# Performance work log

Measured on AMD Instinct MI355X. Metric: run time of the kernel, lower is better.

Reference implementation:

```python
import jax, jax.numpy as jnp
import numpy as np

B, L, D_MODEL = 4, 4096, 128
D_INNER, D_STATE, DT_RANK, D_CONV = 256, 16, 8, 4
EPS = 1e-5


def setup_inputs() -> dict:
    key = jax.random.key(0)
    ks = jax.random.split(key, 10)
    s = lambda *sh: 0.02
    inp = {
        'x': jax.random.normal(ks[0], (B, L, D_MODEL), jnp.float32),
        'norm_w': jnp.ones((D_MODEL,), jnp.float32),
        # Linear weights stored as (in, out) so y = x @ W
        'in_proj_w': jax.random.normal(ks[1], (D_MODEL, 2 * D_INNER), jnp.float32) * 0.02,
        'conv_w': jax.random.normal(ks[2], (D_INNER, D_CONV), jnp.float32) * 0.2,
        'conv_b': jnp.zeros((D_INNER,), jnp.float32),
        'x_proj_w': jax.random.normal(ks[3], (D_INNER, DT_RANK + 2 * D_STATE), jnp.float32) * 0.02,
        'dt_proj_w': jax.random.normal(ks[4], (DT_RANK, D_INNER), jnp.float32) * 0.1,
        'dt_proj_b': jnp.zeros((D_INNER,), jnp.float32),
        'A_log': jnp.log(jnp.tile(jnp.arange(1, D_STATE + 1, dtype=jnp.float32)[None, :], (D_INNER, 1))),
        'D': jnp.ones((D_INNER,), jnp.float32),
        'out_proj_w': jax.random.normal(ks[5], (D_INNER, D_MODEL), jnp.float32) * 0.02,
    }
    return inp


def _mamba_block(x, norm_w, in_proj_w, conv_w, conv_b, x_proj_w,
                 dt_proj_w, dt_proj_b, A_log, D, out_proj_w):
    b, l, d = x.shape
    # RMSNorm
    h = x * jax.lax.rsqrt(jnp.mean(x * x, axis=-1, keepdims=True) + EPS) * norm_w
    # in_proj -> split into x path and residual gate
    xr = h @ in_proj_w                      # (b, l, 2*d_inner)
    xi, res = jnp.split(xr, 2, axis=-1)
    # depthwise causal conv1d over time
    xc = jnp.transpose(xi, (0, 2, 1))       # (b, d_inner, l)
    kernel = conv_w[:, None, :]             # (d_inner, 1, d_conv)
    xc = jax.lax.conv_general_dilated(
        xc, kernel, window_strides=(1,), padding=[(D_CONV - 1, 0)],
        feature_group_count=D_INNER,
        dimension_numbers=('NCH', 'OIH', 'NCH')) + conv_b[None, :, None]
    xc = jnp.transpose(xc, (0, 2, 1))       # (b, l, d_inner)
    xc = jax.nn.silu(xc)
    # SSM parameterization
    A = -jnp.exp(A_log.astype(jnp.float32))           # (d_inner, n)
    x_dbl = xc @ x_proj_w                              # (b, l, dt_rank + 2n)
    delta = x_dbl[..., :DT_RANK]
    Bmat = x_dbl[..., DT_RANK:DT_RANK + D_STATE]       # (b, l, n)
    Cmat = x_dbl[..., DT_RANK + D_STATE:]              # (b, l, n)
    delta = jax.nn.softplus(delta @ dt_proj_w + dt_proj_b)  # (b, l, d_inner)
    # discretize
    deltaA = jnp.exp(jnp.einsum('bld,dn->bldn', delta, A))  # (b, l, d_inner, n)
    deltaB_u = delta[..., None] * Bmat[:, :, None, :] * xc[..., None]
    # selective scan over time (lax.scan replaces the Python loop)
    def step(s, inputs):
        dA_t, dBu_t, C_t = inputs
        s = dA_t * s + dBu_t                     # (b, d_inner, n)
        y_t = jnp.einsum('bdn,bn->bd', s, C_t)   # (b, d_inner)
        return s, y_t
    s0 = jnp.zeros((b, D_INNER, D_STATE), xc.dtype)
    scan_in = (jnp.transpose(deltaA, (1, 0, 2, 3)),
               jnp.transpose(deltaB_u, (1, 0, 2, 3)),
               jnp.transpose(Cmat, (1, 0, 2)))
    _, ys = jax.lax.scan(step, s0, scan_in)      # (l, b, d_inner)
    y = jnp.transpose(ys, (1, 0, 2)) + xc * D    # (b, l, d_inner)
    y = y * jax.nn.silu(res)
    return y @ out_proj_w + x                    # residual add


def reference(x, norm_w, in_proj_w, conv_w, conv_b, x_proj_w,
              dt_proj_w, dt_proj_b, A_log, D, out_proj_w):
    return _mamba_block(x, norm_w, in_proj_w, conv_w, conv_b, x_proj_w,
                        dt_proj_w, dt_proj_b, A_log, D, out_proj_w)
```

## Files before the change

kernel.cpp:

```cpp
#include <hip/hip_runtime.h>
#include <math.h>

#define B_    4
#define L_    4096
#define DM    128
#define DI    256
#define DS    16
#define DTR   8
#define XPN   (DTR + 2*DS)
#define NB    (DI + 2*DS)
#define M_    (B_*L_)
#define CHUNK 32
#define NC    (L_/CHUNK)
#define LOG2E 1.4426950408889634f
#define PREP_N (512*128 + NB*DI + DM*DI)

typedef __attribute__((ext_vector_type(8))) short bf16x8;
typedef __attribute__((ext_vector_type(4))) float f32x4;
typedef unsigned short ushort_t;

__device__ __forceinline__ ushort_t f2bf(float f) {
  unsigned int u = __float_as_uint(f);
  u += 0x7FFFu + ((u >> 16) & 1u);
  return (ushort_t)(u >> 16);
}
__device__ __forceinline__ float bf2f(ushort_t u) {
  return __uint_as_float(((unsigned int)u) << 16);
}

__global__ __launch_bounds__(256) void prep_rms_kernel(const float* __restrict__ x,
                                                       const float* __restrict__ nw,
                                                       const float* __restrict__ inW,
                                                       const float* __restrict__ Wx,
                                                       const float* __restrict__ Wdt,
                                                       const float* __restrict__ outw,
                                                       ushort_t* __restrict__ xbf,
                                                       ushort_t* __restrict__ inWt,
                                                       ushort_t* __restrict__ WbigT,
                                                       ushort_t* __restrict__ outWt) {
  if (blockIdx.x < M_ / 4) {
    int row  = blockIdx.x * 4 + (threadIdx.x >> 6);
    int lane = threadIdx.x & 63;
    const float* xp = x + (size_t)row * DM;
    float v0 = xp[lane], v1 = xp[lane + 64];
    float s = v0 * v0 + v1 * v1;
    #pragma unroll
    for (int off = 32; off > 0; off >>= 1) s += __shfl_xor(s, off);
    float r = rsqrtf(s / DM + 1e-5f);
    ushort_t* op = xbf + (size_t)row * DM;
    op[lane]      = f2bf(v0 * r * nw[lane]);
    op[lane + 64] = f2bf(v1 * r * nw[lane + 64]);
    return;
  }
  int g = (blockIdx.x - M_ / 4) * 256 + threadIdx.x;
  if (g < 512 * 128) {
    int n = g >> 7, k = g & 127;
    inWt[g] = f2bf(inW[k * 512 + n]);
  } else if (g < 512 * 128 + NB * DI) {
    int q = g - 512 * 128;
    int c = q >> 8, k = q & 255;
    float v;
    if (c < DI) {
      v = 0.f;
      #pragma unroll
      for (int j = 0; j < DTR; ++j) v = fmaf(Wx[k * XPN + j], Wdt[j * DI + c], v);
    } else {
      v = Wx[k * XPN + DTR + (c - DI)];
    }
    WbigT[q] = f2bf(v);
  } else if (g < PREP_N) {
    int q = g - (512 * 128 + NB * DI);
    int n = q >> 8, k = q & 255;
    outWt[q] = f2bf(outw[k * DM + n]);
  }
}

__global__ __launch_bounds__(256) void g1_conv_kernel(const ushort_t* __restrict__ A,
                                                      const ushort_t* __restrict__ Wt,
                                                      const float* __restrict__ cw,
                                                      const float* __restrict__ cb,
                                                      ushort_t* __restrict__ xcbf,
                                                      ushort_t* __restrict__ resbf) {
  constexpr int KK = 128, NT = 4;
  __shared__ __align__(16) char smem_raw[35648];
  ushort_t (*Asm)[145][8] = (ushort_t (*)[145][8])smem_raw;
  ushort_t (*Bx)[65][8]   = (ushort_t (*)[65][8])(smem_raw + 18560);
  ushort_t (*Br)[65][8]   = (ushort_t (*)[65][8])(smem_raw + 26880);
  float* T = (float*)smem_raw;
  const int tid  = threadIdx.x;
  const int wave = tid >> 6, lane = tid & 63;
  const int quad = lane >> 4, l16 = lane & 15;
  const int row0 = blockIdx.x * 128;
  const int by   = blockIdx.y;
  const int c0x  = by * 64;
  const int c0r  = 256 + by * 64;
  const bool zpad = (row0 & (L_ - 1)) == 0;
  f32x4 ax[2][NT], ar[2][NT], acc2[NT];
  #pragma unroll
  for (int mt = 0; mt < 2; ++mt)
    #pragma unroll
    for (int nt = 0; nt < NT; ++nt) {
      ax[mt][nt] = (f32x4){0.f, 0.f, 0.f, 0.f};
      ar[mt][nt] = (f32x4){0.f, 0.f, 0.f, 0.f};
    }
  #pragma unroll
  for (int nt = 0; nt < NT; ++nt) acc2[nt] = (f32x4){0.f, 0.f, 0.f, 0.f};

  for (int k0 = 0; k0 < KK; k0 += 64) {
    #pragma unroll
    for (int i = 0; i < 5; ++i) {
      int q = tid + i * 256;
      if (i < 4 || tid < 128) {
        int m = q >> 3, kb = q & 7;
        bf16x8 v = {0, 0, 0, 0, 0, 0, 0, 0};
        if (!(zpad && m < 16))
          v = *(const bf16x8*)(A + (size_t)(row0 - 16 + m) * KK + k0 + kb * 8);
        *(bf16x8*)(&Asm[kb][m][0]) = v;
      }
    }
    #pragma unroll
    for (int i = 0; i < 2; ++i) {
      int q = tid + i * 256;
      int n = q >> 3, kb = q & 7;
      *(bf16x8*)(&Bx[kb][n][0]) =
          *(const bf16x8*)(Wt + (size_t)(c0x + n) * KK + k0 + kb * 8);
    }
    #pragma unroll
    for (int i = 0; i < 2; ++i) {
      int q = tid + i * 256;
      int n = q >> 3, kb = q & 7;
      *(bf16x8*)(&Br[kb][n][0]) =
          *(const bf16x8*)(Wt + (size_t)(c0r + n) * KK + k0 + kb * 8);
    }
    __syncthreads();
    #pragma unroll
    for (int ks = 0; ks < 2; ++ks) {
      bf16x8 af[2], bx[NT], br[NT];
      #pragma unroll
      for (int mt = 0; mt < 2; ++mt)
        af[mt] = *(const bf16x8*)(&Asm[ks * 4 + quad][16 + wave * 32 + mt * 16 + l16][0]);
      #pragma unroll
      for (int nt = 0; nt < NT; ++nt) {
        bx[nt] = *(const bf16x8*)(&Bx[ks * 4 + quad][nt * 16 + l16][0]);
        br[nt] = *(const bf16x8*)(&Br[ks * 4 + quad][nt * 16 + l16][0]);
      }
      #pragma unroll
      for (int mt = 0; mt < 2; ++mt)
        #pragma unroll
        for (int nt = 0; nt < NT; ++nt) {
          ax[mt][nt] = __builtin_amdgcn_mfma_f32_16x16x32_bf16(af[mt], bx[nt],
                                                               ax[mt][nt], 0, 0, 0);
          ar[mt][nt] = __builtin_amdgcn_mfma_f32_16x16x32_bf16(af[mt], br[nt],
                                                               ar[mt][nt], 0, 0, 0);
        }
      if (wave == 0) {
        bf16x8 ab = *(const bf16x8*)(&Asm[ks * 4 + quad][l16][0]);
        #pragma unroll
        for (int nt = 0; nt < NT; ++nt)
          acc2[nt] = __builtin_amdgcn_mfma_f32_16x16x32_bf16(ab, bx[nt],
                                                             acc2[nt], 0, 0, 0);
      }
    }
    __syncthreads();
  }

  #pragma unroll
  for (int mt = 0; mt < 2; ++mt)
    #pragma unroll
    for (int nt = 0; nt < NT; ++nt) {
      int col   = c0x + nt * 16 + l16;
      int rbase = row0 + wave * 32 + mt * 16 + quad * 4;
      #pragma unroll
      for (int r = 0; r < 4; ++r)
        resbf[(size_t)(rbase + r) * DI + col] = f2bf(ar[mt][nt][r]);
    }

  #pragma unroll
  for (int mt = 0; mt < 2; ++mt)
    #pragma unroll
    for (int nt = 0; nt < NT; ++nt)
      #pragma unroll
      for (int r = 0; r < 4; ++r)
        T[(3 + wave * 32 + mt * 16 + quad * 4 + r) * 68 + nt * 16 + l16] =
            ax[mt][nt][r];
  if (wave == 0 && quad == 3) {
    #pragma unroll
    for (int nt = 0; nt < NT; ++nt)
      #pragma unroll
      for (int r = 1; r < 4; ++r)
        T[(r - 1) * 68 + nt * 16 + l16] = acc2[nt][r];
  }
  __syncthreads();
  {
    const int c   = tid & 63;
    const int R0  = (tid >> 6) * 32;
    const int dch = c0x + c;
    float4 w4   = *(const float4*)(cw + dch * 4);
    float bias  = cb[dch];
    float t0 = T[(R0 + 0) * 68 + c];
    float t1 = T[(R0 + 1) * 68 + c];
    float t2 = T[(R0 + 2) * 68 + c];
    for (int rr = 0; rr < 32; ++rr) {
      float t3 = T[(R0 + rr + 3) * 68 + c];
      float s = fmaf(w4.x, t0, fmaf(w4.y, t1, fmaf(w4.z, t2, fmaf(w4.w, t3, bias))));
      float v = s / (1.f + __expf(-s));
      xcbf[(size_t)(row0 + R0 + rr) * DI + dch] = f2bf(v);
      t0 = t1; t1 = t2; t2 = t3;
    }
  }
}

__global__ __launch_bounds__(512, 4) void scanA_kernel(
    const ushort_t* __restrict__ xcbf, const ushort_t* __restrict__ WbigT,
    const float* __restrict__ bdt, const float* __restrict__ Alog,
    ushort_t* __restrict__ deltab, ushort_t* __restrict__ Bmb,
    ushort_t* __restrict__ Cmb, float2* __restrict__ PS) {
  __shared__ __align__(16) ushort_t Asm[32][33][8];
  __shared__ float T[32][257];
  __shared__ float Bs[32][17], Cs[32][17];
  const int tid  = threadIdx.x;
  const int wave = tid >> 6, lane = tid & 63;
  const int quad = lane >> 4, l16 = lane & 15;
  const int b = blockIdx.x >> 7, c = blockIdx.x & (NC - 1);
  const size_t rowbase = (size_t)b * L_ + (size_t)c * CHUNK;
  const int d  = (wave << 5) | (lane & 31);
  const int nh = lane >> 5;
  const int n0 = nh * 8;

  {
    int m = tid & 31, kb = tid >> 5;
    *(bf16x8*)(&Asm[kb][m][0]) =
        *(const bf16x8*)(xcbf + (rowbase + m) * DI + kb * 8);
    *(bf16x8*)(&Asm[kb + 16][m][0]) =
        *(const bf16x8*)(xcbf + (rowbase + m) * DI + (kb + 16) * 8);
  }
  __syncthreads();

  for (int tp = wave; tp < 36; tp += 8) {
    int mt = tp / 18, nt = tp % 18;
    f32x4 acc = {0.f, 0.f, 0.f, 0.f};
    #pragma unroll
    for (int ks = 0; ks < 8; ++ks) {
      bf16x8 af = *(const bf16x8*)(&Asm[ks * 4 + quad][mt * 16 + l16][0]);
      bf16x8 bf = *(const bf16x8*)(WbigT + (size_t)(nt * 16 + l16) * DI + ks * 32 + quad * 8);
      acc = __builtin_amdgcn_mfma_f32_16x16x32_bf16(af, bf, acc, 0, 0, 0);
    }
    int row = mt * 16 + quad * 4;
    if (nt < 16) {
      int col = nt * 16 + l16;
      float bb = bdt[col];
      #pragma unroll
      for (int r = 0; r < 4; ++r) {
        float v = acc[r] + bb;
        T[row + r][col] = (v > 20.f) ? v : log1pf(__expf(v));
      }
    } else if (nt == 16) {
      #pragma unroll
      for (int r = 0; r < 4; ++r) Bs[row + r][l16] = acc[r];
    } else {
      #pragma unroll
      for (int r = 0; r < 4; ++r) Cs[row + r][l16] = acc[r];
    }
  }
  __syncthreads();

  #pragma unroll
  for (int i = 0; i < 8; ++i) {
    int idx2 = tid + i * 512;
    int row = idx2 >> 7, cp = idx2 & 127;
    unsigned int pk = (unsigned int)f2bf(T[row][2 * cp]) |
                      ((unsigned int)f2bf(T[row][2 * cp + 1]) << 16);
    *(unsigned int*)(deltab + (rowbase + row) * DI + 2 * cp) = pk;
  }
  {
    int row = tid >> 4, n = tid & 15;
    Bmb[rowbase * DS + tid] = f2bf(Bs[row][n]);
    Cmb[rowbase * DS + tid] = f2bf(Cs[row][n]);
  }

  float c0 = -__expf(Alog[d * DS]) * LOG2E;
  float aln[8];
  #pragma unroll
  for (int j = 0; j < 8; ++j) aln[j] = -__expf(Alog[d * DS + n0 + j]) * LOG2E;
  bool geom = true;
  #pragma unroll
  for (int j = 0; j < 8; ++j)
    geom = geom && (fabsf(aln[j] - (n0 + j + 1) * c0) <= 1e-3f * fabsf(aln[j]));

  float P[8], S[8];
  #pragma unroll
  for (int j = 0; j < 8; ++j) { P[j] = 1.f; S[j] = 0.f; }
  for (int t = 0; t < CHUNK; ++t) {
    float dl = T[t][d];
    float xv = bf2f(Asm[d >> 3][t][d & 7]);
    float du = dl * xv;
    if (geom) {
      float e1 = exp2f(dl * c0);
      float a;
      if (nh) { float e2 = e1 * e1, e4 = e2 * e2; a = e4 * e4 * e1; }
      else a = e1;
      #pragma unroll
      for (int j = 0; j < 8; ++j) {
        P[j] *= a;
        S[j] = fmaf(a, S[j], du * Bs[t][n0 + j]);
        a *= e1;
      }
    } else {
      #pragma unroll
      for (int j = 0; j < 8; ++j) {
        float a = exp2f(dl * aln[j]);
        P[j] *= a;
        S[j] = fmaf(a, S[j], du * Bs[t][n0 + j]);
      }
    }
  }
  size_t ob = ((size_t)(b * NC + c) << 12) + ((nh * 256 + d) << 3);
  float4* p4 = (float4*)(PS + ob);
  p4[0] = make_float4(P[0], S[0], P[1], S[1]);
  p4[1] = make_float4(P[2], S[2], P[3], S[3]);
  p4[2] = make_float4(P[4], S[4], P[5], S[5]);
  p4[3] = make_float4(P[6], S[6], P[7], S[7]);
}

__global__ __launch_bounds__(64) void scanB_kernel(const float2* __restrict__ PS,
                                                   float* __restrict__ sinit) {
  int g  = blockIdx.x * 64 + threadIdx.x;
  int b  = g >> 12;
  int dn = g & 4095;
  float s = 0.f;
  #pragma unroll 16
  for (int c = 0; c < NC; ++c) {
    size_t idx = ((size_t)(b * NC + c) << 12) + dn;
    sinit[idx] = s;
    float2 v = PS[idx];
    s = fmaf(v.x, s, v.y);
  }
}

__global__ __launch_bounds__(512, 4) void scanC_kernel(
    const ushort_t* __restrict__ deltab, const ushort_t* __restrict__ xcbf,
    const ushort_t* __restrict__ Bmb, const ushort_t* __restrict__ Cmb,
    const float* __restrict__ Alog, const float* __restrict__ Dp,
    const ushort_t* __restrict__ resbf, const float* __restrict__ sinit,
    const ushort_t* __restrict__ outWt, const float* __restrict__ x,
    float* __restrict__ out) {
  __shared__ float Bs[32][17], Cs[32][17];
  __shared__ __align__(16) ushort_t y2s[32][264];
  const int tid  = threadIdx.x;
  const int wave = tid >> 6, lane = tid & 63;
  const int quad = lane >> 4, l16 = lane & 15;
  const int b = blockIdx.x >> 7, c = blockIdx.x & (NC - 1);
  const size_t rowbase = (size_t)b * L_ + (size_t)c * CHUNK;
  const int d  = (wave << 5) | (lane & 31);
  const int nh = lane >> 5;
  const int n0 = nh * 8;
  {
    int row = tid >> 4, n = tid & 15;
    Bs[row][n] = bf2f(Bmb[rowbase * DS + tid]);
    Cs[row][n] = bf2f(Cmb[rowbase * DS + tid]);
  }
  float c0 = -__expf(Alog[d * DS]) * LOG2E;
  float aln[8];
  #pragma unroll
  for (int j = 0; j < 8; ++j) aln[j] = -__expf(Alog[d * DS + n0 + j]) * LOG2E;
  bool geom = true;
  #pragma unroll
  for (int j = 0; j < 8; ++j)
    geom = geom && (fabsf(aln[j] - (n0 + j + 1) * c0) <= 1e-3f * fabsf(aln[j]));
  const float Dd = Dp[d];
  float S[8];
  {
    size_t ib = ((size_t)(b * NC + c) << 12) + ((nh * 256 + d) << 3);
    float4 v0 = *(const float4*)(sinit + ib);
    float4 v1 = *(const float4*)(sinit + ib + 4);
    S[0] = v0.x; S[1] = v0.y; S[2] = v0.z; S[3] = v0.w;
    S[4] = v1.x; S[5] = v1.y; S[6] = v1.z; S[7] = v1.w;
  }
  __syncthreads();
  for (int t = 0; t < CHUNK; ++t) {
    float dl = bf2f(deltab[(rowbase + t) * DI + d]);
    float xv = bf2f(xcbf[(rowbase + t) * DI + d]);
    float du = dl * xv;
    float y = 0.f;
    if (geom) {
      float e1 = exp2f(dl * c0);
      float a;
      if (nh) { float e2 = e1 * e1, e4 = e2 * e2; a = e4 * e4 * e1; }
      else a = e1;
      #pragma unroll
      for (int j = 0; j < 8; ++j) {
        S[j] = fmaf(a, S[j], du * Bs[t][n0 + j]);
        y = fmaf(S[j], Cs[t][n0 + j], y);
        a *= e1;
      }
    } else {
      #pragma unroll
      for (int j = 0; j < 8; ++j) {
        float a = exp2f(dl * aln[j]);
        S[j] = fmaf(a, S[j], du * Bs[t][n0 + j]);
        y = fmaf(S[j], Cs[t][n0 + j], y);
      }
    }
    float yo = __shfl_xor(y, 32);
    if (nh == 0) {
      float rv = bf2f(resbf[(rowbase + t) * DI + d]);
      float yt = y + yo + xv * Dd;
      float sil = rv / (1.f + __expf(-rv));
      y2s[t][d] = f2bf(yt * sil);
    }
  }
  __syncthreads();
  #pragma unroll
  for (int mt = 0; mt < 2; ++mt) {
    f32x4 acc = {0.f, 0.f, 0.f, 0.f};
    #pragma unroll
    for (int ks = 0; ks < 8; ++ks) {
      bf16x8 af = *(const bf16x8*)(&y2s[mt * 16 + l16][ks * 32 + quad * 8]);
      bf16x8 bf = *(const bf16x8*)(outWt + (size_t)(wave * 16 + l16) * DI + ks * 32 + quad * 8);
      acc = __builtin_amdgcn_mfma_f32_16x16x32_bf16(af, bf, acc, 0, 0, 0);
    }
    int col = wave * 16 + l16;
    size_t rb = rowbase + mt * 16 + quad * 4;
    #pragma unroll
    for (int r = 0; r < 4; ++r)
      out[(rb + r) * DM + col] = acc[r] + x[(rb + r) * DM + col];
  }
}

extern "C" void kernel_launch(void* const* d_in, const int* in_sizes, int n_in,
                              void* d_out, int out_size, void* d_ws, size_t ws_size,
                              hipStream_t stream) {
  const float* x      = (const float*)d_in[0];
  const float* norm_w = (const float*)d_in[1];
  const float* inW    = (const float*)d_in[2];
  const float* convw  = (const float*)d_in[3];
  const float* convb  = (const float*)d_in[4];
  const float* xprojw = (const float*)d_in[5];
  const float* dtw    = (const float*)d_in[6];
  const float* dtb    = (const float*)d_in[7];
  const float* alog   = (const float*)d_in[8];
  const float* Dp     = (const float*)d_in[9];
  const float* outw   = (const float*)d_in[10];
  float* out = (float*)d_out;

  const size_t CS = (size_t)B_ * NC * DI * DS;
  float2* PS    = (float2*)d_ws;
  float* sinit  = (float*)(PS + CS);
  ushort_t* bfbase = (ushort_t*)(sinit + CS);
  ushort_t* xbf    = bfbase;
  ushort_t* xcbf   = xbf + (size_t)M_ * DM;
  ushort_t* resbf  = xcbf + (size_t)M_ * DI;
  ushort_t* deltab = resbf + (size_t)M_ * DI;
  ushort_t* Bmb    = deltab + (size_t)M_ * DI;
  ushort_t* Cmb    = Bmb + (size_t)M_ * DS;
  ushort_t* inWt   = Cmb + (size_t)M_ * DS;
  ushort_t* WbigT  = inWt + 512 * 128;
  ushort_t* outWt  = WbigT + NB * DI;

  prep_rms_kernel<<<M_ / 4 + (PREP_N + 255) / 256, 256, 0, stream>>>(
      x, norm_w, inW, xprojw, dtw, outw, xbf, inWt, WbigT, outWt);
  g1_conv_kernel<<<dim3(M_ / 128, 4), 256, 0, stream>>>(
      xbf, inWt, convw, convb, xcbf, resbf);
  scanA_kernel<<<B_ * NC, 512, 0, stream>>>(
      xcbf, WbigT, dtb, alog, deltab, Bmb, Cmb, PS);
  scanB_kernel<<<(B_ * DI * DS) / 64, 64, 0, stream>>>(PS, sinit);
  scanC_kernel<<<B_ * NC, 512, 0, stream>>>(
      deltab, xcbf, Bmb, Cmb, alog, Dp, resbf, sinit, outWt, x, out);
}
```

Baseline: 170.0 us.

## Parallelize inter-chunk state scan and vectorize B/C shared-memory reads

The inter-chunk carry kernel changes from a serial 128-step loop per (batch, state) thread to a two-level scan. Each of 16 segments first reduces 8 chunks, then a Hillis-Steele scan over the segments runs in shared memory, and the segment-local prefixes are written back. This shortens the serial dependency chain and raises occupancy, in exchange for extra syncs. Separately, the B and C shared arrays are padded to 20 columns so each thread can load its 8 values with two float4 reads per timestep instead of scalar reads.

```diff
diff --git a/kernel.cpp b/kernel.cpp
--- a/kernel.cpp
+++ b/kernel.cpp
@@ -217,7 +217,7 @@
     ushort_t* __restrict__ Cmb, float2* __restrict__ PS) {
   __shared__ __align__(16) ushort_t Asm[32][33][8];
   __shared__ float T[32][257];
-  __shared__ float Bs[32][17], Cs[32][17];
+  __shared__ float Bs[32][20], Cs[32][20];
   const int tid  = threadIdx.x;
   const int wave = tid >> 6, lane = tid & 63;
   const int quad = lane >> 4, l16 = lane & 15;
@@ -294,6 +294,9 @@
     float dl = T[t][d];
     float xv = bf2f(Asm[d >> 3][t][d & 7]);
     float du = dl * xv;
+    float Bv[8];
+    *(float4*)&Bv[0] = *(const float4*)&Bs[t][n0];
+    *(float4*)&Bv[4] = *(const float4*)&Bs[t][n0 + 4];
     if (geom) {
       float e1 = exp2f(dl * c0);
       float a;
@@ -302,7 +305,7 @@
       #pragma unroll
       for (int j = 0; j < 8; ++j) {
         P[j] *= a;
-        S[j] = fmaf(a, S[j], du * Bs[t][n0 + j]);
+        S[j] = fmaf(a, S[j], du * Bv[j]);
         a *= e1;
       }
     } else {
@@ -310,7 +313,7 @@
       for (int j = 0; j < 8; ++j) {
         float a = exp2f(dl * aln[j]);
         P[j] *= a;
-        S[j] = fmaf(a, S[j], du * Bs[t][n0 + j]);
+        S[j] = fmaf(a, S[j], du * Bv[j]);
       }
     }
   }
@@ -322,18 +325,42 @@
   p4[3] = make_float4(P[6], S[6], P[7], S[7]);
 }
 
-__global__ __launch_bounds__(64) void scanB_kernel(const float2* __restrict__ PS,
-                                                   float* __restrict__ sinit) {
-  int g  = blockIdx.x * 64 + threadIdx.x;
-  int b  = g >> 12;
-  int dn = g & 4095;
-  float s = 0.f;
-  #pragma unroll 16
-  for (int c = 0; c < NC; ++c) {
-    size_t idx = ((size_t)(b * NC + c) << 12) + dn;
-    sinit[idx] = s;
-    float2 v = PS[idx];
-    s = fmaf(v.x, s, v.y);
+__global__ __launch_bounds__(1024) void scanB_kernel(const float2* __restrict__ PS,
+                                                     float* __restrict__ sinit) {
+  __shared__ float Ps[16][64], Ss[16][64];
+  const int tid = threadIdx.x;
+  const int seg = tid >> 6;
+  const int j   = tid & 63;
+  const int b   = blockIdx.x >> 6;
+  const int dn  = ((blockIdx.x & 63) << 6) + j;
+  const size_t base = ((size_t)(b * NC + seg * 8) << 12) + (size_t)dn;
+  float Pk[8], Sk[8];
+  #pragma unroll
+  for (int k = 0; k < 8; ++k) {
+    float2 v = PS[base + ((size_t)k << 12)];
+    Pk[k] = v.x; Sk[k] = v.y;
+  }
+  float Pg = 1.f, Sg = 0.f;
+  #pragma unroll
+  for (int k = 0; k < 8; ++k) { Sg = fmaf(Pk[k], Sg, Sk[k]); Pg *= Pk[k]; }
+  Ps[seg][j] = Pg; Ss[seg][j] = Sg;
+  __syncthreads();
+  #pragma unroll
+  for (int off = 1; off < 16; off <<= 1) {
+    float Pp = 1.f, Sp = 0.f;
+    if (seg >= off) { Pp = Ps[seg - off][j]; Sp = Ss[seg - off][j]; }
+    __syncthreads();
+    if (seg >= off) {
+      Sg = fmaf(Pg, Sp, Sg); Pg *= Pp;
+      Ps[seg][j] = Pg; Ss[seg][j] = Sg;
+    }
+    __syncthreads();
+  }
+  float s = (seg == 0) ? 0.f : Ss[seg - 1][j];
+  #pragma unroll
+  for (int k = 0; k < 8; ++k) {
+    sinit[base + ((size_t)k << 12)] = s;
+    s = fmaf(Pk[k], s, Sk[k]);
   }
 }
 
@@ -344,7 +371,7 @@
     const ushort_t* __restrict__ resbf, const float* __restrict__ sinit,
     const ushort_t* __restrict__ outWt, const float* __restrict__ x,
     float* __restrict__ out) {
-  __shared__ float Bs[32][17], Cs[32][17];
+  __shared__ float Bs[32][20], Cs[32][20];
   __shared__ __align__(16) ushort_t y2s[32][264];
   const int tid  = threadIdx.x;
   const int wave = tid >> 6, lane = tid & 63;
@@ -381,6 +408,11 @@
     float dl = bf2f(deltab[(rowbase + t) * DI + d]);
     float xv = bf2f(xcbf[(rowbase + t) * DI + d]);
     float du = dl * xv;
+    float Bv[8], Cv[8];
+    *(float4*)&Bv[0] = *(const float4*)&Bs[t][n0];
+    *(float4*)&Bv[4] = *(const float4*)&Bs[t][n0 + 4];
+    *(float4*)&Cv[0] = *(const float4*)&Cs[t][n0];
+    *(float4*)&Cv[4] = *(const float4*)&Cs[t][n0 + 4];
     float y = 0.f;
     if (geom) {
       float e1 = exp2f(dl * c0);
@@ -389,16 +421,16 @@
       else a = e1;
       #pragma unroll
       for (int j = 0; j < 8; ++j) {
-        S[j] = fmaf(a, S[j], du * Bs[t][n0 + j]);
-        y = fmaf(S[j], Cs[t][n0 + j], y);
+        S[j] = fmaf(a, S[j], du * Bv[j]);
+        y = fmaf(S[j], Cv[j], y);
         a *= e1;
       }
     } else {
       #pragma unroll
       for (int j = 0; j < 8; ++j) {
         float a = exp2f(dl * aln[j]);
-        S[j] = fmaf(a, S[j], du * Bs[t][n0 + j]);
-        y = fmaf(S[j], Cs[t][n0 + j], y);
+        S[j] = fmaf(a, S[j], du * Bv[j]);
+        y = fmaf(S[j], Cv[j], y);
       }
     }
     float yo = __shfl_xor(y, 32);
@@ -463,7 +495,7 @@
       xbf, inWt, convw, convb, xcbf, resbf);
   scanA_kernel<<<B_ * NC, 512, 0, stream>>>(
       xcbf, WbigT, dtb, alog, deltab, Bmb, Cmb, PS);
-  scanB_kernel<<<(B_ * DI * DS) / 64, 64, 0, stream>>>(PS, sinit);
+  scanB_kernel<<<B_ * 64, 1024, 0, stream>>>(PS, sinit);
   scanC_kernel<<<B_ * NC, 512, 0, stream>>>(
       deltab, xcbf, Bmb, Cmb, alog, Dp, resbf, sinit, outWt, x, out);
 }
```

New measurement: 165.8 us. 2.5% less time.
